# Optimization experiments

Measured on AMD Instinct MI355X. Metric: run time of the kernel, lower is better.

Reference implementation:

```python
import jax, jax.numpy as jnp
import numpy as np

B, N = 8, 128          # batch, nodes
D = 256                # message_size (== resized node/edge feature size)
LH = 512               # link_hidden_size
P = 3                  # propagate_layers
C = 117                # hoi_classes
DE, DN = 200, 100      # raw edge / node feature sizes


def setup_inputs() -> dict:
    key = jax.random.key(0)
    ks = jax.random.split(key, 12)
    g = lambda k, sh, s=0.05: jax.random.normal(k, sh, dtype=jnp.float32) * s
    return {
        "edge_features": jax.random.normal(ks[0], (B, N, N, DE), dtype=jnp.float32),
        "node_features": jax.random.normal(ks[1], (B, N, DN), dtype=jnp.float32),
        # feature resize linears
        "W_er": g(ks[2], (D, DE)), "b_er": jnp.zeros((D,), jnp.float32),
        "W_nr": g(ks[3], (D, DN)), "b_nr": jnp.zeros((D,), jnp.float32),
        # link function: GraphConv = per-edge MLP (1x1 convs), last layer -> 1 channel
        "Wl1": g(ks[4], (LH, D)), "bl1": jnp.zeros((LH,), jnp.float32),
        "Wl2": g(ks[5], (LH, LH)), "bl2": jnp.zeros((LH,), jnp.float32),
        "Wl3": g(ks[6], (1, LH)), "bl3": jnp.zeros((1,), jnp.float32),
        # message function: Linear(concat(h_w, e_vw)) + ReLU
        "W_m": g(ks[7], (D, 2 * D)), "b_m": jnp.zeros((D,), jnp.float32),
        # GRU update (single layer): torch GRU weight layout [r; z; n]
        "W_ih": g(ks[8], (3 * D, D)), "b_ih": jnp.zeros((3 * D,), jnp.float32),
        "W_hh": g(ks[9], (3 * D, D)), "b_hh": jnp.zeros((3 * D,), jnp.float32),
        # readout fc
        "W_r": g(ks[10], (C, D)), "b_r": jnp.zeros((C,), jnp.float32),
    }


def reference(edge_features, node_features, W_er, b_er, W_nr, b_nr,
              Wl1, bl1, Wl2, bl2, Wl3, bl3, W_m, b_m,
              W_ih, b_ih, W_hh, b_hh, W_r, b_r):
    # resize raw features to message size
    ef = edge_features @ W_er.T + b_er           # [B,N_i,N_w,D] (target i, source w)
    h = node_features @ W_nr.T + b_nr            # [B,N,D] node hidden states

    e_state = ef                                  # hidden edge state fed to link fun
    pred_adj = None
    for _ in range(P):
        # link function: per-edge MLP (equivalent to 1x1 Conv2d stack), 1-channel out
        x = jax.nn.relu(e_state @ Wl1.T + bl1)
        x = jax.nn.relu(x @ Wl2.T + bl2)
        pred_adj = (x @ Wl3.T + bl3)[..., 0]      # [B,N,N] pre-sigmoid adjacency
        sig = jax.nn.sigmoid(pred_adj)

        # messages m(i<-w) = relu(Linear([h_w ; e_{i,w}])), gated by sigmoid adj
        hw = jnp.broadcast_to(h[:, None, :, :], ef.shape)  # [B,N_i,N_w,D]
        M = jax.nn.relu(jnp.concatenate([hw, ef], axis=-1) @ W_m.T + b_m)
        M = sig[..., None] * M                    # [B,N_i,N_w,D]

        # torch code writes m_v into hidden_edge_states[...][:, :, :, i] -> transpose (i,w)
        e_state = jnp.transpose(M, (0, 2, 1, 3))

        # aggregate over sources, GRU single-step update (input=m, hidden=h)
        m = M.sum(axis=2)                         # [B,N,D]
        gi = m @ W_ih.T + b_ih
        gh = h @ W_hh.T + b_hh
        r = jax.nn.sigmoid(gi[..., :D] + gh[..., :D])
        z = jax.nn.sigmoid(gi[..., D:2 * D] + gh[..., D:2 * D])
        n = jnp.tanh(gi[..., 2 * D:] + r * gh[..., 2 * D:])
        h = (1.0 - z) * n + z * h

    pred_node_labels = h @ W_r.T + b_r            # [B,N,C]
    return pred_adj, pred_node_labels
```

## Files before the change

kernel.cpp:

```cpp
#include <hip/hip_runtime.h>
#include <math.h>

typedef unsigned short u16;
typedef __attribute__((ext_vector_type(8))) short short8;
typedef __attribute__((ext_vector_type(4))) short short4v;
typedef __attribute__((ext_vector_type(4))) float floatx4;

__device__ __forceinline__ float bf2f(u16 u) {
  union { unsigned int i; float f; } v; v.i = ((unsigned int)u) << 16; return v.f;
}
__device__ __forceinline__ u16 f2bf(float f) {
  union { unsigned int i; float f; } v; v.f = f;
  unsigned int i = v.i;
  unsigned int lsb = (i >> 16) & 1u;
  i += 0x7fffu + lsb;
  return (u16)(i >> 16);
}

__global__ __launch_bounds__(256, 2)
void fused_front_k(const float* __restrict__ edge, const u16* __restrict__ Wcomb,
                   const float* __restrict__ b_er, const float* __restrict__ cmb,
                   u16* __restrict__ es, u16* __restrict__ Em)
{
  __shared__ __align__(16) u16 As[64 * 232];
  const int tid  = threadIdx.x;
  const int lane = tid & 63;
  const int wv   = tid >> 6;
  const int q    = lane >> 4;
  const int cl   = lane & 15;
  const long r0  = (long)blockIdx.x * 64;

  for (int z = tid; z < 64 * 24; z += 256) {
    const int zr = z / 24;
    As[zr * 232 + 200 + (z - zr * 24)] = 0;
  }
  const float4* src = (const float4*)(edge + r0 * 200);
  for (int it = tid; it < 3200; it += 256) {
    const float4 v = src[it];
    const int row = it / 50;
    const int c4  = it - row * 50;
    u16 t[4] = { f2bf(v.x), f2bf(v.y), f2bf(v.z), f2bf(v.w) };
    *(short4v*)&As[row * 232 + c4 * 4] = *(short4v*)t;
  }
  __syncthreads();

  floatx4 acc[8][4];
#pragma unroll
  for (int wi = 0; wi < 8; ++wi)
#pragma unroll
    for (int ri = 0; ri < 4; ++ri)
      acc[wi][ri] = (floatx4){0.f, 0.f, 0.f, 0.f};

  short8 b0[8], b1[8];
#pragma unroll
  for (int wi = 0; wi < 8; ++wi)
    b0[wi] = *(const short8*)(Wcomb + (long)(wv * 128 + wi * 16 + cl) * 224 + q * 8);
#pragma unroll
  for (int ks = 0; ks < 7; ++ks) {
    short8* bc = (ks & 1) ? b1 : b0;
    short8* bn = (ks & 1) ? b0 : b1;
    if (ks < 6) {
      const int kb = (ks + 1) * 32;
#pragma unroll
      for (int wi = 0; wi < 8; ++wi)
        bn[wi] = *(const short8*)(Wcomb + (long)(wv * 128 + wi * 16 + cl) * 224 + kb + q * 8);
    }
    short8 a[4];
#pragma unroll
    for (int ri = 0; ri < 4; ++ri)
      a[ri] = *(const short8*)&As[(ri * 16 + cl) * 232 + ks * 32 + q * 8];
#pragma unroll
    for (int wi = 0; wi < 8; ++wi)
#pragma unroll
      for (int ri = 0; ri < 4; ++ri)
        acc[wi][ri] = __builtin_amdgcn_mfma_f32_16x16x32_bf16(bc[wi], a[ri], acc[wi][ri], 0, 0, 0);
  }

  const bool is_ef   = (wv < 2);
  const float* bias  = is_ef ? b_er : cmb;
  u16* dst           = is_ef ? es : Em;
  const int colbase  = (wv & 1) * 128;
#pragma unroll
  for (int wi = 0; wi < 8; ++wi) {
    const int c0i = colbase + wi * 16 + q * 4;
    const float4 bv = *(const float4*)&bias[c0i];
    const float bb[4] = {bv.x, bv.y, bv.z, bv.w};
#pragma unroll
    for (int ri = 0; ri < 4; ++ri) {
      const int row = ri * 16 + cl;
      u16 p[4];
#pragma unroll
      for (int r = 0; r < 4; ++r)
        p[r] = f2bf(acc[wi][ri][r] + bb[r]);
      *(short4v*)&dst[(r0 + row) * 256 + c0i] = *(short4v*)p;
    }
  }
}

__global__ __launch_bounds__(512, 2)
void linkmsg_k(const u16* __restrict__ es, const u16* __restrict__ Wl1b,
               const float* __restrict__ bl1, const u16* __restrict__ Wl2b,
               const float* __restrict__ bl2, const float* __restrict__ wl3,
               const float* __restrict__ bl3, const u16* __restrict__ Em,
               const float* __restrict__ Hm, float* __restrict__ adj,
               u16* __restrict__ esn, float* __restrict__ msum,
               const int write_adj, const int write_es)
{
  __shared__ __align__(16) u16 x1b[128 * 512];
  const int tid  = threadIdx.x;
  const int lane = tid & 63;
  const int wv   = tid >> 6;
  const int q    = lane >> 4;
  const int cl   = lane & 15;
  const int nw0  = wv * 64;
  const long r0  = (long)blockIdx.x * 128;

  {
    const short8* gsrc = (const short8*)(es + r0 * 256);
#pragma unroll
    for (int i = 0; i < 8; ++i) {
      const int g   = tid + i * 512;
      const int row = g >> 5;
      const int c   = g & 31;
      const short8 v = gsrc[g];
      *(short8*)&x1b[row * 256 + ((c ^ (row & 15)) << 3)] = v;
    }
  }

  floatx4 acc[4][8];
#pragma unroll
  for (int ni = 0; ni < 4; ++ni)
#pragma unroll
    for (int mi = 0; mi < 8; ++mi)
      acc[ni][mi] = (floatx4){0.f, 0.f, 0.f, 0.f};

  short8 b0[4], b1[4];
#pragma unroll
  for (int ni = 0; ni < 4; ++ni)
    b0[ni] = *(const short8*)(Wl1b + (nw0 + ni * 16 + cl) * 256 + q * 8);
  __syncthreads();

  {
#pragma unroll
    for (int ks = 0; ks < 8; ++ks) {
      short8* bc = (ks & 1) ? b1 : b0;
      short8* bn = (ks & 1) ? b0 : b1;
      if (ks < 7) {
        const int kb = (ks + 1) * 32;
#pragma unroll
        for (int ni = 0; ni < 4; ++ni)
          bn[ni] = *(const short8*)(Wl1b + (nw0 + ni * 16 + cl) * 256 + kb + q * 8);
      }
      short8 a[8];
#pragma unroll
      for (int mi = 0; mi < 8; ++mi) {
        const int row = mi * 16 + cl;
        a[mi] = *(const short8*)&x1b[row * 256 + (((ks * 4 + q) ^ cl) << 3)];
      }
#pragma unroll
      for (int ni = 0; ni < 4; ++ni)
#pragma unroll
        for (int mi = 0; mi < 8; ++mi)
          acc[ni][mi] = __builtin_amdgcn_mfma_f32_16x16x32_bf16(bc[ni], a[mi], acc[ni][mi], 0, 0, 0);
    }
  }
  __syncthreads();

  {
#pragma unroll
    for (int ni = 0; ni < 4; ++ni) {
      const int ocb   = nw0 + ni * 16 + q * 4;
      const float4 bv = *(const float4*)&bl1[ocb];
      const float bb[4] = {bv.x, bv.y, bv.z, bv.w};
      const int chunk = ocb >> 3;
      const int off   = ocb & 7;
#pragma unroll
      for (int mi = 0; mi < 8; ++mi) {
        const int row = mi * 16 + cl;
        u16 p[4];
#pragma unroll
        for (int r = 0; r < 4; ++r)
          p[r] = f2bf(fmaxf(acc[ni][mi][r] + bb[r], 0.f));
        *(short4v*)&x1b[row * 512 + ((chunk ^ cl) << 3) + off] = *(short4v*)p;
      }
    }
  }
#pragma unroll
  for (int ni = 0; ni < 4; ++ni)
#pragma unroll
    for (int mi = 0; mi < 8; ++mi)
      acc[ni][mi] = (floatx4){0.f, 0.f, 0.f, 0.f};
  __syncthreads();

  {
    short8 c0[4], c1[4];
#pragma unroll
    for (int ni = 0; ni < 4; ++ni)
      c0[ni] = *(const short8*)(Wl2b + (nw0 + ni * 16 + cl) * 512 + q * 8);
#pragma unroll
    for (int ks = 0; ks < 16; ++ks) {
      short8* cc = (ks & 1) ? c1 : c0;
      short8* cn = (ks & 1) ? c0 : c1;
      if (ks < 15) {
        const int kb = (ks + 1) * 32;
#pragma unroll
        for (int ni = 0; ni < 4; ++ni)
          cn[ni] = *(const short8*)(Wl2b + (nw0 + ni * 16 + cl) * 512 + kb + q * 8);
      }
      short8 a[8];
#pragma unroll
      for (int mi = 0; mi < 8; ++mi) {
        const int row = mi * 16 + cl;
        a[mi] = *(const short8*)&x1b[row * 512 + (((ks * 4 + q) ^ cl) << 3)];
      }
#pragma unroll
      for (int ni = 0; ni < 4; ++ni)
#pragma unroll
        for (int mi = 0; mi < 8; ++mi)
          acc[ni][mi] = __builtin_amdgcn_mfma_f32_16x16x32_bf16(cc[ni], a[mi], acc[ni][mi], 0, 0, 0);
    }
  }

  float pv[8];
#pragma unroll
  for (int mi = 0; mi < 8; ++mi) pv[mi] = 0.f;
#pragma unroll
  for (int ni = 0; ni < 4; ++ni) {
    const int ocb   = nw0 + ni * 16 + q * 4;
    const float4 b2 = *(const float4*)&bl2[ocb];
    const float4 w3 = *(const float4*)&wl3[ocb];
    const float bb[4] = {b2.x, b2.y, b2.z, b2.w};
    const float ww[4] = {w3.x, w3.y, w3.z, w3.w};
#pragma unroll
    for (int mi = 0; mi < 8; ++mi) {
#pragma unroll
      for (int r = 0; r < 4; ++r)
        pv[mi] += fmaxf(acc[ni][mi][r] + bb[r], 0.f) * ww[r];
    }
  }
  __syncthreads();
  float* pf   = (float*)x1b;
  float* sigv = pf + 1024;
  float* red  = pf + 2048;
#pragma unroll
  for (int mi = 0; mi < 8; ++mi) {
    float p = pv[mi];
    p += __shfl_xor(p, 16, 64);
    p += __shfl_xor(p, 32, 64);
    if (q == 0) pf[wv * 128 + mi * 16 + cl] = p;
  }
  __syncthreads();
  if (tid < 128) {
    float s = bl3[0];
#pragma unroll
    for (int w = 0; w < 8; ++w) s += pf[w * 128 + tid];
    if (write_adj) adj[r0 + tid] = s;
    sigv[tid] = 1.f / (1.f + __expf(-s));
  }
  __syncthreads();

  const int b  = (int)(blockIdx.x >> 7);
  const int i  = (int)(blockIdx.x & 127);
  const int g  = tid >> 5;
  const int c8 = (tid & 31) * 8;
  float msacc[8] = {0.f, 0.f, 0.f, 0.f, 0.f, 0.f, 0.f, 0.f};
  for (int w0 = 0; w0 < 128; w0 += 16) {
    const int w = w0 + g;
    const float s = sigv[w];
    const short8 ev = *(const short8*)(Em + (r0 + w) * 256 + c8);
    const float4 h0 = *(const float4*)(Hm + ((long)(b * 128 + w)) * 256 + c8);
    const float4 h1 = *(const float4*)(Hm + ((long)(b * 128 + w)) * 256 + c8 + 4);
    const float hv[8] = {h0.x, h0.y, h0.z, h0.w, h1.x, h1.y, h1.z, h1.w};
    u16 mb[8];
#pragma unroll
    for (int j = 0; j < 8; ++j) {
      float x = fmaxf(bf2f(((const u16*)&ev)[j]) + hv[j], 0.f) * s;
      msacc[j] += x;
      mb[j] = f2bf(x);
    }
    if (write_es)
      *(short8*)(esn + (((long)(b * 128 + w)) * 128 + i) * 256 + c8) = *(short8*)mb;
  }
  {
    float4 m0 = {msacc[0], msacc[1], msacc[2], msacc[3]};
    float4 m1 = {msacc[4], msacc[5], msacc[6], msacc[7]};
    *(float4*)&red[tid * 8]     = m0;
    *(float4*)&red[tid * 8 + 4] = m1;
  }
  __syncthreads();
  if (tid < 256) {
    float s = 0.f;
#pragma unroll
    for (int gg = 0; gg < 16; ++gg) s += red[gg * 256 + tid];
    msum[((long)(b * 128 + i)) * 256 + tid] = s;
  }
}

__device__ __forceinline__
void gemm_sp_dev(const float* __restrict__ A, const u16* __restrict__ Bh,
                 const u16* __restrict__ Bl, const float* __restrict__ bias,
                 float* __restrict__ C,
                 int N, int K_loop, int K_src, int lda, int ldc,
                 int bx, int by)
{
  __shared__ __align__(16) u16 Ash[128 * 40];
  __shared__ __align__(16) u16 Asl[128 * 40];
  __shared__ __align__(16) u16 Bsh[128 * 40];
  __shared__ __align__(16) u16 Bsl[128 * 40];
  const int tid  = threadIdx.x;
  const int m0   = bx * 128;
  const int n0   = by * 128;
  const int lane = tid & 63;
  const int wv   = tid >> 6;
  const int wm   = wv & 1;
  const int wn   = wv >> 1;
  const int q    = lane >> 4;
  const int cl   = lane & 15;

  floatx4 acc[4][4];
#pragma unroll
  for (int i = 0; i < 4; ++i)
#pragma unroll
    for (int j = 0; j < 4; ++j)
      acc[i][j] = (floatx4){0.f, 0.f, 0.f, 0.f};

  const int srow = tid >> 1;
  const int scol = (tid & 1) * 16;

  for (int kb = 0; kb < K_loop; kb += 32) {
    {
      const long r = (long)(m0 + srow);
      u16* dh = &Ash[srow * 40 + scol];
      u16* dl = &Asl[srow * 40 + scol];
#pragma unroll
      for (int j = 0; j < 16; ++j) {
        int kg = kb + scol + j;
        float v = (kg < K_src) ? A[r * lda + kg] : 0.f;
        u16 hi = f2bf(v);
        dh[j] = hi;
        dl[j] = f2bf(v - bf2f(hi));
      }
    }
    {
      const int n = n0 + srow;
      u16* dh = &Bsh[srow * 40 + scol];
      u16* dl = &Bsl[srow * 40 + scol];
      if (n < N) {
        const short8* sh = (const short8*)(Bh + (long)n * K_loop + kb + scol);
        const short8* sl = (const short8*)(Bl + (long)n * K_loop + kb + scol);
        ((short8*)dh)[0] = sh[0]; ((short8*)dh)[1] = sh[1];
        ((short8*)dl)[0] = sl[0]; ((short8*)dl)[1] = sl[1];
      } else {
#pragma unroll
        for (int j = 0; j < 16; ++j) { dh[j] = 0; dl[j] = 0; }
      }
    }
    __syncthreads();

    short8 ah[4], al[4], bh[4], bl[4];
#pragma unroll
    for (int mi = 0; mi < 4; ++mi) {
      ah[mi] = *(const short8*)&Ash[(wm * 64 + mi * 16 + cl) * 40 + q * 8];
      al[mi] = *(const short8*)&Asl[(wm * 64 + mi * 16 + cl) * 40 + q * 8];
    }
#pragma unroll
    for (int ni = 0; ni < 4; ++ni) {
      bh[ni] = *(const short8*)&Bsh[(wn * 64 + ni * 16 + cl) * 40 + q * 8];
      bl[ni] = *(const short8*)&Bsl[(wn * 64 + ni * 16 + cl) * 40 + q * 8];
    }
#pragma unroll
    for (int mi = 0; mi < 4; ++mi)
#pragma unroll
      for (int ni = 0; ni < 4; ++ni) {
        acc[mi][ni] = __builtin_amdgcn_mfma_f32_16x16x32_bf16(ah[mi], bh[ni], acc[mi][ni], 0, 0, 0);
        acc[mi][ni] = __builtin_amdgcn_mfma_f32_16x16x32_bf16(al[mi], bh[ni], acc[mi][ni], 0, 0, 0);
        acc[mi][ni] = __builtin_amdgcn_mfma_f32_16x16x32_bf16(ah[mi], bl[ni], acc[mi][ni], 0, 0, 0);
      }
    __syncthreads();
  }

#pragma unroll
  for (int mi = 0; mi < 4; ++mi) {
    const int row = m0 + wm * 64 + mi * 16 + q * 4;
#pragma unroll
    for (int ni = 0; ni < 4; ++ni) {
      const int col = n0 + wn * 64 + ni * 16 + cl;
      if (col < N) {
        const float b = bias ? bias[col] : 0.f;
#pragma unroll
        for (int r = 0; r < 4; ++r) {
          float v = acc[mi][ni][r] + b;
          C[(long)(row + r) * ldc + col] = v;
        }
      }
    }
  }
}

__global__ __launch_bounds__(256, 2)
void gemm_sp_k(const float* __restrict__ A, const u16* __restrict__ Bh,
               const u16* __restrict__ Bl, const float* __restrict__ bias,
               float* __restrict__ C,
               int N, int K_loop, int K_src, int lda, int ldc)
{
  gemm_sp_dev(A, Bh, Bl, bias, C, N, K_loop, K_src, lda, ldc,
              blockIdx.x, blockIdx.y);
}

__global__ __launch_bounds__(256, 2)
void gemm_hm_gh_k(const float* __restrict__ hbuf,
                  const u16* __restrict__ Wmh_h, const u16* __restrict__ Wmh_l,
                  const u16* __restrict__ Whh_h, const u16* __restrict__ Whh_l,
                  const float* __restrict__ b_hh,
                  float* __restrict__ Hm, float* __restrict__ gh)
{
  if (blockIdx.z == 0) {
    if (blockIdx.y >= 2) return;
    gemm_sp_dev(hbuf, Wmh_h, Wmh_l, nullptr, Hm, 256, 256, 256, 256, 256,
                blockIdx.x, blockIdx.y);
  } else {
    gemm_sp_dev(hbuf, Whh_h, Whh_l, b_hh, gh, 768, 256, 256, 256, 768,
                blockIdx.x, blockIdx.y);
  }
}

__device__ __forceinline__
void cast_pad_dev(u16* __restrict__ dst, const float* __restrict__ src,
                  int rows, int sc, int dc, int stride, int idx)
{
  if (idx >= rows * dc) return;
  int r = idx / dc, c = idx - r * dc;
  float v = (c < sc) ? src[r * stride + c] : 0.f;
  dst[idx] = f2bf(v);
}

__device__ __forceinline__
void cast_split_dev(u16* __restrict__ dh, u16* __restrict__ dl,
                    const float* __restrict__ src,
                    int rows, int sc, int dc, int stride, int idx)
{
  if (idx >= rows * dc) return;
  int r = idx / dc, c = idx - r * dc;
  float v = (c < sc) ? src[r * stride + c] : 0.f;
  u16 hi = f2bf(v);
  dh[idx] = hi;
  dl[idx] = f2bf(v - bf2f(hi));
}

__global__ __launch_bounds__(256)
void prep_all_k(const float* __restrict__ W_er, const float* __restrict__ Wl1,
                const float* __restrict__ Wl2, const float* __restrict__ W_nr,
                const float* __restrict__ W_m, const float* __restrict__ W_ih,
                const float* __restrict__ W_hh, const float* __restrict__ W_r,
                const float* __restrict__ b_er, const float* __restrict__ b_m,
                u16* __restrict__ Wcomb, u16* __restrict__ Wl1b,
                u16* __restrict__ Wl2b,
                u16* __restrict__ Wnr_h, u16* __restrict__ Wnr_l,
                u16* __restrict__ Wmh_h, u16* __restrict__ Wmh_l,
                u16* __restrict__ Wih_h, u16* __restrict__ Wih_l,
                u16* __restrict__ Whh_h, u16* __restrict__ Whh_l,
                u16* __restrict__ Wr_h, u16* __restrict__ Wr_l,
                float* __restrict__ cmb)
{
  const int j = blockIdx.y;
  if (j == 8) {
    if (blockIdx.x >= 256) return;
    const int o = blockIdx.x;
    const int t = threadIdx.x;
    __shared__ float wme[256];
    wme[t] = W_m[o * 512 + 256 + t];
    __syncthreads();
    if (t < 224) {
      float s = 0.f;
      if (t < 200) {
        for (int c = 0; c < 256; ++c) s += wme[c] * W_er[c * 200 + t];
      }
      Wcomb[(256 + o) * 224 + t] = f2bf(s);
    }
    if (t == 0) {
      float s = 0.f;
      for (int c = 0; c < 256; ++c) s += wme[c] * b_er[c];
      cmb[o] = s + b_m[o];
    }
    return;
  }
  const int idx = blockIdx.x * 256 + threadIdx.x;
  switch (j) {
    case 0: cast_pad_dev(Wcomb, W_er, 256, 200, 224, 200, idx); break;
    case 1: cast_pad_dev(Wl1b, Wl1, 512, 256, 256, 256, idx); break;
    case 2: cast_pad_dev(Wl2b, Wl2, 512, 512, 512, 512, idx); break;
    case 3: cast_split_dev(Wnr_h, Wnr_l, W_nr, 256, 100, 128, 100, idx); break;
    case 4: cast_split_dev(Wmh_h, Wmh_l, W_m, 256, 256, 256, 512, idx); break;
    case 5: cast_split_dev(Wih_h, Wih_l, W_ih, 768, 256, 256, 256, idx); break;
    case 6: cast_split_dev(Whh_h, Whh_l, W_hh, 768, 256, 256, 256, idx); break;
    case 7: cast_split_dev(Wr_h, Wr_l, W_r, 117, 256, 256, 256, idx); break;
  }
}

__global__ void gru_k(const float* __restrict__ gi, const float* __restrict__ gh,
                      float* __restrict__ h)
{
  const int n = blockIdx.x;
  const int d = threadIdx.x;
  const int base = n * 768;
  const float r  = 1.f / (1.f + __expf(-(gi[base + d] + gh[base + d])));
  const float z  = 1.f / (1.f + __expf(-(gi[base + 256 + d] + gh[base + 256 + d])));
  const float nn = tanhf(gi[base + 512 + d] + r * gh[base + 512 + d]);
  const int hi = n * 256 + d;
  h[hi] = (1.f - z) * nn + z * h[hi];
}

extern "C" void kernel_launch(void* const* d_in, const int* in_sizes, int n_in,
                              void* d_out, int out_size, void* d_ws, size_t ws_size,
                              hipStream_t stream)
{
  const float* edge = (const float*)d_in[0];
  const float* node = (const float*)d_in[1];
  const float* W_er = (const float*)d_in[2];
  const float* b_er = (const float*)d_in[3];
  const float* W_nr = (const float*)d_in[4];
  const float* b_nr = (const float*)d_in[5];
  const float* Wl1  = (const float*)d_in[6];
  const float* bl1  = (const float*)d_in[7];
  const float* Wl2  = (const float*)d_in[8];
  const float* bl2  = (const float*)d_in[9];
  const float* Wl3  = (const float*)d_in[10];
  const float* bl3  = (const float*)d_in[11];
  const float* W_m  = (const float*)d_in[12];
  const float* b_m  = (const float*)d_in[13];
  const float* W_ih = (const float*)d_in[14];
  const float* b_ih = (const float*)d_in[15];
  const float* W_hh = (const float*)d_in[16];
  const float* b_hh = (const float*)d_in[17];
  const float* W_r  = (const float*)d_in[18];
  const float* b_r  = (const float*)d_in[19];
  (void)in_sizes; (void)n_in; (void)out_size; (void)ws_size;

  float* out_adj = (float*)d_out;
  float* out_lab = (float*)d_out + 131072;

  char* ws = (char*)d_ws;
  size_t off = 0;
  auto alloc = [&](size_t bytes) -> void* {
    void* p = ws + off; off += (bytes + 255) & ~(size_t)255; return p;
  };
  const long E = 131072;
  u16*   es0  = (u16*)  alloc(E * 256 * 2);
  u16*   es1  = (u16*)  alloc(E * 256 * 2);
  u16*   Em   = (u16*)  alloc(E * 256 * 2);
  float* Hm   = (float*)alloc(1024 * 256 * 4);
  float* hbuf = (float*)alloc(1024 * 256 * 4);
  float* msum = (float*)alloc(1024 * 256 * 4);
  float* gi   = (float*)alloc(1024 * 768 * 4);
  float* gh   = (float*)alloc(1024 * 768 * 4);
  u16*   Wcomb = (u16*) alloc(512 * 224 * 2);
  u16*   Wl1b = (u16*)  alloc(512 * 256 * 2);
  u16*   Wl2b = (u16*)  alloc(512 * 512 * 2);
  float* cmb  = (float*)alloc(256 * 4);
  u16* Wnr_h = (u16*)alloc(256 * 128 * 2); u16* Wnr_l = (u16*)alloc(256 * 128 * 2);
  u16* Wmh_h = (u16*)alloc(256 * 256 * 2); u16* Wmh_l = (u16*)alloc(256 * 256 * 2);
  u16* Wih_h = (u16*)alloc(768 * 256 * 2); u16* Wih_l = (u16*)alloc(768 * 256 * 2);
  u16* Whh_h = (u16*)alloc(768 * 256 * 2); u16* Whh_l = (u16*)alloc(768 * 256 * 2);
  u16* Wr_h  = (u16*)alloc(117 * 256 * 2); u16* Wr_l  = (u16*)alloc(117 * 256 * 2);

  prep_all_k<<<dim3(1024, 9), 256, 0, stream>>>(
      W_er, Wl1, Wl2, W_nr, W_m, W_ih, W_hh, W_r, b_er, b_m,
      Wcomb, Wl1b, Wl2b, Wnr_h, Wnr_l, Wmh_h, Wmh_l,
      Wih_h, Wih_l, Whh_h, Whh_l, Wr_h, Wr_l, cmb);

  fused_front_k<<<2048, dim3(256), 0, stream>>>(edge, Wcomb, b_er, cmb, es0, Em);
  gemm_sp_k<<<dim3(8, 2), dim3(256), 0, stream>>>(
      node, Wnr_h, Wnr_l, b_nr, hbuf, 256, 128, 100, 100, 256);

  u16* esbuf[2] = { es0, es1 };
  for (int p = 0; p < 3; ++p) {
    gemm_hm_gh_k<<<dim3(8, 6, 2), dim3(256), 0, stream>>>(
        hbuf, Wmh_h, Wmh_l, Whh_h, Whh_l, b_hh, Hm, gh);
    linkmsg_k<<<1024, dim3(512), 0, stream>>>(
        esbuf[p & 1], Wl1b, bl1, Wl2b, bl2, Wl3, bl3,
        Em, Hm, out_adj, esbuf[(p + 1) & 1], msum,
        (p == 2) ? 1 : 0, (p < 2) ? 1 : 0);
    gemm_sp_k<<<dim3(8, 6), dim3(256), 0, stream>>>(
        msum, Wih_h, Wih_l, b_ih, gi, 768, 256, 256, 256, 768);
    gru_k<<<1024, 256, 0, stream>>>(gi, gh, hbuf);
  }
  gemm_sp_k<<<dim3(8, 1), dim3(256), 0, stream>>>(
      hbuf, Wr_h, Wr_l, b_r, out_lab, 117, 256, 256, 256, 117);
}
```

Measured before the change: 907.9 us.

## Fuse input-gate GEMM with GRU update, add MFMA priority hints, compact hm/gh grid

Replaces the separate W_ih GEMM plus elementwise GRU kernel with one kernel that computes the r/z/n gate tiles for a column slice and applies the GRU update in the epilogue. This removes the gi buffer round-trip and one launch per propagation step. It also wraps the MFMA inner loops of the front and link kernels in s_setprio raises, and reshapes the hm/gh grid so no blocks exit idle. The new fused GEMM uses a small tile with split-bf16 three-pass MFMA and no double buffering, so its efficiency may be lower than the old GEMM.

```diff
diff --git a/kernel.cpp b/kernel.cpp
--- a/kernel.cpp
+++ b/kernel.cpp
@@ -69,11 +69,13 @@
 #pragma unroll
     for (int ri = 0; ri < 4; ++ri)
       a[ri] = *(const short8*)&As[(ri * 16 + cl) * 232 + ks * 32 + q * 8];
+    __builtin_amdgcn_s_setprio(1);
 #pragma unroll
     for (int wi = 0; wi < 8; ++wi)
 #pragma unroll
       for (int ri = 0; ri < 4; ++ri)
         acc[wi][ri] = __builtin_amdgcn_mfma_f32_16x16x32_bf16(bc[wi], a[ri], acc[wi][ri], 0, 0, 0);
+    __builtin_amdgcn_s_setprio(0);
   }
 
   const bool is_ef   = (wv < 2);
@@ -157,11 +159,13 @@
         const int row = mi * 16 + cl;
         a[mi] = *(const short8*)&x1b[row * 256 + (((ks * 4 + q) ^ cl) << 3)];
       }
+      __builtin_amdgcn_s_setprio(1);
 #pragma unroll
       for (int ni = 0; ni < 4; ++ni)
 #pragma unroll
         for (int mi = 0; mi < 8; ++mi)
           acc[ni][mi] = __builtin_amdgcn_mfma_f32_16x16x32_bf16(bc[ni], a[mi], acc[ni][mi], 0, 0, 0);
+      __builtin_amdgcn_s_setprio(0);
     }
   }
   __syncthreads();
@@ -213,11 +217,13 @@
         const int row = mi * 16 + cl;
         a[mi] = *(const short8*)&x1b[row * 512 + (((ks * 4 + q) ^ cl) << 3)];
       }
+      __builtin_amdgcn_s_setprio(1);
 #pragma unroll
       for (int ni = 0; ni < 4; ++ni)
 #pragma unroll
         for (int mi = 0; mi < 8; ++mi)
           acc[ni][mi] = __builtin_amdgcn_mfma_f32_16x16x32_bf16(cc[ni], a[mi], acc[ni][mi], 0, 0, 0);
+      __builtin_amdgcn_s_setprio(0);
     }
   }
 
@@ -414,14 +420,118 @@
                   const float* __restrict__ b_hh,
                   float* __restrict__ Hm, float* __restrict__ gh)
 {
-  if (blockIdx.z == 0) {
-    if (blockIdx.y >= 2) return;
+  const int y = blockIdx.y;
+  if (y < 2) {
     gemm_sp_dev(hbuf, Wmh_h, Wmh_l, nullptr, Hm, 256, 256, 256, 256, 256,
-                blockIdx.x, blockIdx.y);
+                blockIdx.x, y);
   } else {
     gemm_sp_dev(hbuf, Whh_h, Whh_l, b_hh, gh, 768, 256, 256, 256, 768,
-                blockIdx.x, blockIdx.y);
-  }
+                blockIdx.x, y - 2);
+  }
+}
+
+__global__ __launch_bounds__(256, 2)
+void gemm_gru_k(const float* __restrict__ A,
+                const u16* __restrict__ Bh, const u16* __restrict__ Bl,
+                const float* __restrict__ b_ih,
+                const float* __restrict__ gh,
+                float* __restrict__ h)
+{
+  __shared__ __align__(16) u16 Ash[64 * 40];
+  __shared__ __align__(16) u16 Asl[64 * 40];
+  __shared__ __align__(16) u16 Bsh[192 * 40];
+  __shared__ __align__(16) u16 Bsl[192 * 40];
+  const int tid  = threadIdx.x;
+  const int m0   = blockIdx.x * 64;
+  const int cb   = blockIdx.y * 64;
+  const int lane = tid & 63;
+  const int wv   = tid >> 6;
+  const int wm   = wv & 1;
+  const int wn   = wv >> 1;
+  const int q    = lane >> 4;
+  const int cl   = lane & 15;
+
+  floatx4 acc[3][2][2];
+#pragma unroll
+  for (int g = 0; g < 3; ++g)
+#pragma unroll
+    for (int mi = 0; mi < 2; ++mi)
+#pragma unroll
+      for (int ni = 0; ni < 2; ++ni)
+        acc[g][mi][ni] = (floatx4){0.f, 0.f, 0.f, 0.f};
+
+  const int arow = tid >> 2;
+  const int acol = (tid & 3) * 8;
+
+  for (int kb = 0; kb < 256; kb += 32) {
+    {
+      const float* ap = A + (long)(m0 + arow) * 256 + kb + acol;
+      u16* dh = &Ash[arow * 40 + acol];
+      u16* dl = &Asl[arow * 40 + acol];
+#pragma unroll
+      for (int j = 0; j < 8; ++j) {
+        float v = ap[j];
+        u16 hi = f2bf(v);
+        dh[j] = hi;
+        dl[j] = f2bf(v - bf2f(hi));
+      }
+    }
+    for (int s = tid; s < 384; s += 256) {
+      const int br = s >> 1;
+      const int bc = (s & 1) * 16;
+      const int g  = br >> 6;
+      const int r  = br & 63;
+      const long wrow = (long)(g * 256 + cb + r);
+      *(short8*)&Bsh[br * 40 + bc]     = *(const short8*)(Bh + wrow * 256 + kb + bc);
+      *(short8*)&Bsh[br * 40 + bc + 8] = *(const short8*)(Bh + wrow * 256 + kb + bc + 8);
+      *(short8*)&Bsl[br * 40 + bc]     = *(const short8*)(Bl + wrow * 256 + kb + bc);
+      *(short8*)&Bsl[br * 40 + bc + 8] = *(const short8*)(Bl + wrow * 256 + kb + bc + 8);
+    }
+    __syncthreads();
+
+    short8 ah[2], al[2];
+#pragma unroll
+    for (int mi = 0; mi < 2; ++mi) {
+      ah[mi] = *(const short8*)&Ash[(wm * 32 + mi * 16 + cl) * 40 + q * 8];
+      al[mi] = *(const short8*)&Asl[(wm * 32 + mi * 16 + cl) * 40 + q * 8];
+    }
+#pragma unroll
+    for (int g = 0; g < 3; ++g)
+#pragma unroll
+      for (int ni = 0; ni < 2; ++ni) {
+        const short8 bh = *(const short8*)&Bsh[(g * 64 + wn * 32 + ni * 16 + cl) * 40 + q * 8];
+        const short8 bl = *(const short8*)&Bsl[(g * 64 + wn * 32 + ni * 16 + cl) * 40 + q * 8];
+#pragma unroll
+        for (int mi = 0; mi < 2; ++mi) {
+          acc[g][mi][ni] = __builtin_amdgcn_mfma_f32_16x16x32_bf16(ah[mi], bh, acc[g][mi][ni], 0, 0, 0);
+          acc[g][mi][ni] = __builtin_amdgcn_mfma_f32_16x16x32_bf16(al[mi], bh, acc[g][mi][ni], 0, 0, 0);
+          acc[g][mi][ni] = __builtin_amdgcn_mfma_f32_16x16x32_bf16(ah[mi], bl, acc[g][mi][ni], 0, 0, 0);
+        }
+      }
+    __syncthreads();
+  }
+
+#pragma unroll
+  for (int mi = 0; mi < 2; ++mi)
+#pragma unroll
+    for (int ni = 0; ni < 2; ++ni) {
+      const int col = cb + wn * 32 + ni * 16 + cl;
+      const float bi_r = b_ih[col];
+      const float bi_z = b_ih[256 + col];
+      const float bi_n = b_ih[512 + col];
+#pragma unroll
+      for (int r = 0; r < 4; ++r) {
+        const int row = m0 + wm * 32 + mi * 16 + q * 4 + r;
+        const long gb = (long)row * 768;
+        const float gr = (acc[0][mi][ni][r] + bi_r) + gh[gb + col];
+        const float gz = (acc[1][mi][ni][r] + bi_z) + gh[gb + 256 + col];
+        const float rv = 1.f / (1.f + __expf(-gr));
+        const float zv = 1.f / (1.f + __expf(-gz));
+        const float nv = tanhf((acc[2][mi][ni][r] + bi_n) + rv * gh[gb + 512 + col]);
+        const int hidx = row * 256 + col;
+        h[hidx] = (1.f - zv) * nv + zv * h[hidx];
+      }
+    }
 }
 
 __device__ __forceinline__
@@ -495,19 +605,6 @@
     case 6: cast_split_dev(Whh_h, Whh_l, W_hh, 768, 256, 256, 256, idx); break;
     case 7: cast_split_dev(Wr_h, Wr_l, W_r, 117, 256, 256, 256, idx); break;
   }
-}
-
-__global__ void gru_k(const float* __restrict__ gi, const float* __restrict__ gh,
-                      float* __restrict__ h)
-{
-  const int n = blockIdx.x;
-  const int d = threadIdx.x;
-  const int base = n * 768;
-  const float r  = 1.f / (1.f + __expf(-(gi[base + d] + gh[base + d])));
-  const float z  = 1.f / (1.f + __expf(-(gi[base + 256 + d] + gh[base + 256 + d])));
-  const float nn = tanhf(gi[base + 512 + d] + r * gh[base + 512 + d]);
-  const int hi = n * 256 + d;
-  h[hi] = (1.f - z) * nn + z * h[hi];
 }
 
 extern "C" void kernel_launch(void* const* d_in, const int* in_sizes, int n_in,
@@ -551,7 +648,6 @@
   float* Hm   = (float*)alloc(1024 * 256 * 4);
   float* hbuf = (float*)alloc(1024 * 256 * 4);
   float* msum = (float*)alloc(1024 * 256 * 4);
-  float* gi   = (float*)alloc(1024 * 768 * 4);
   float* gh   = (float*)alloc(1024 * 768 * 4);
   u16*   Wcomb = (u16*) alloc(512 * 224 * 2);
   u16*   Wl1b = (u16*)  alloc(512 * 256 * 2);
@@ -574,15 +670,14 @@
 
   u16* esbuf[2] = { es0, es1 };
   for (int p = 0; p < 3; ++p) {
-    gemm_hm_gh_k<<<dim3(8, 6, 2), dim3(256), 0, stream>>>(
+    gemm_hm_gh_k<<<dim3(8, 8), dim3(256), 0, stream>>>(
         hbuf, Wmh_h, Wmh_l, Whh_h, Whh_l, b_hh, Hm, gh);
     linkmsg_k<<<1024, dim3(512), 0, stream>>>(
         esbuf[p & 1], Wl1b, bl1, Wl2b, bl2, Wl3, bl3,
         Em, Hm, out_adj, esbuf[(p + 1) & 1], msum,
         (p == 2) ? 1 : 0, (p < 2) ? 1 : 0);
-    gemm_sp_k<<<dim3(8, 6), dim3(256), 0, stream>>>(
-        msum, Wih_h, Wih_l, b_ih, gi, 768, 256, 256, 256, 768);
-    gru_k<<<1024, 256, 0, stream>>>(gi, gh, hbuf);
+    gemm_gru_k<<<dim3(16, 4), dim3(256), 0, stream>>>(
+        msum, Wih_h, Wih_l, b_ih, gh, hbuf);
   }
   gemm_sp_k<<<dim3(8, 1), dim3(256), 0, stream>>>(
       hbuf, Wr_h, Wr_l, b_r, out_lab, 117, 256, 256, 256, 117);
```

Measured after the change: 847.3 us. 6.7% less time.
